# Kernel optimization log

Hardware: AMD Instinct MI355X
Metric: run time of the kernel (lower is better)

The kernel has to match this reference:

```python
import jax, jax.numpy as jnp
import numpy as np


def setup_inputs() -> dict:
    key = jax.random.key(0)
    k1, k2 = jax.random.split(key, 2)
    B, N, D = 8, 2048, 1024
    x = jax.random.normal(k1, (B, N, D), dtype=jnp.float32)
    # Linear(D, 3D): weight stored as [in, out] for x @ W
    W_qkv = jax.random.normal(k2, (D, 3 * D), dtype=jnp.float32) * (D ** -0.5)
    b_qkv = jnp.zeros((3 * D,), dtype=jnp.float32)
    return {"x": x, "W_qkv": W_qkv, "b_qkv": b_qkv}


def reference(x, W_qkv, b_qkv):
    D = x.shape[-1]
    scale = D ** -0.5
    qkv = x @ W_qkv + b_qkv                      # [B, N, 3D]
    q, k, v = jnp.split(qkv, 3, axis=-1)         # each [B, N, D]
    # attention scores: note original scales AFTER matmul (same math)
    atten = jnp.einsum('bnd,bmd->bnm', q, k) * scale  # [B, N, N]
    atten = jax.nn.softmax(atten, axis=-1)
    out = jnp.einsum('bnm,bmd->bnd', atten, v)   # [B, N, D]
    return out
```

## Files before the change

### kernel.cpp

```cpp
#include <hip/hip_runtime.h>
#include <hip/hip_bf16.h>


typedef __attribute__((ext_vector_type(8))) short bf16x8;
typedef __attribute__((ext_vector_type(4))) float f32x4;
typedef __attribute__((ext_vector_type(8))) unsigned short u16x8;
typedef __attribute__((address_space(1))) const unsigned int gu32;
typedef __attribute__((address_space(3))) unsigned int lu32;

__device__ __forceinline__ unsigned short f2bf(float f) {
  union { float f; unsigned int u; } v; v.f = f;
  unsigned int r = v.u + 0x7fffu + ((v.u >> 16) & 1u);
  return (unsigned short)(r >> 16);
}
__device__ __forceinline__ void cp16(const unsigned short* g, unsigned short* l) {
  __builtin_amdgcn_global_load_lds((gu32*)g, (lu32*)l, 16, 0, 0);
}

__global__ __launch_bounds__(256) void prep(const float* __restrict__ x,
                                            unsigned short* __restrict__ xb,
                                            const float* __restrict__ W,
                                            unsigned short* __restrict__ Wt,
                                            float* __restrict__ rowsum) {
  __shared__ unsigned short tile[64][72];
  int bid = blockIdx.x, t = threadIdx.x;
  if (bid < 8192) {
    long i = ((long)bid * 256 + t) * 8;
    float4 a = *(const float4*)(x + i);
    float4 b = *(const float4*)(x + i + 4);
    u16x8 o;
    o[0] = f2bf(a.x); o[1] = f2bf(a.y); o[2] = f2bf(a.z); o[3] = f2bf(a.w);
    o[4] = f2bf(b.x); o[5] = f2bf(b.y); o[6] = f2bf(b.z); o[7] = f2bf(b.w);
    *(u16x8*)(xb + i) = o;
  } else if (bid < 8960) {
    int wb = bid - 8192;
    int fb = wb % 48, db = wb / 48;
#pragma unroll
    for (int it = 0; it < 4; it++) {
      int c = t + it * 256;
      int r = c >> 4, c4 = (c & 15) * 4;
      float4 v = *(const float4*)(W + (long)(db * 64 + r) * 3072 + fb * 64 + c4);
      tile[r][c4 + 0] = f2bf(v.x); tile[r][c4 + 1] = f2bf(v.y);
      tile[r][c4 + 2] = f2bf(v.z); tile[r][c4 + 3] = f2bf(v.w);
    }
    __syncthreads();
#pragma unroll
    for (int it = 0; it < 2; it++) {
      int c = t + it * 256;
      int r2 = c >> 3, k8 = (c & 7) * 8;
      u16x8 o;
#pragma unroll
      for (int j = 0; j < 8; j++) o[j] = tile[k8 + j][r2];
      *(u16x8*)(Wt + (long)(fb * 64 + r2) * 1024 + db * 64 + k8) = o;
    }
  } else {
    rowsum[(bid - 8960) * 256 + t] = 0.f;
  }
}

template <int MODE, int SWZ>
__global__ __launch_bounds__(512, 2) void gemm256(
    const unsigned short* __restrict__ A, const unsigned short* __restrict__ B,
    float* __restrict__ C, const float* __restrict__ bias, int Ncols, int K, float scale,
    unsigned short* __restrict__ qp, unsigned short* __restrict__ kp,
    unsigned short* __restrict__ vp, float* __restrict__ rsum,
    long strA, long strB, long strC) {
  __shared__ __align__(16) unsigned short As[2][256 * 64];
  __shared__ __align__(16) unsigned short Bs[2][256 * 64];
  const int tid = threadIdx.x;
  const int lane = tid & 63, wave = tid >> 6;
  const int quad = lane >> 4, l16 = lane & 15;
  const int lr = lane >> 3, lc = lane & 7;
  const int bz = blockIdx.z;
  int mt, nt;
  if (SWZ == 0) {
    mt = blockIdx.y; nt = blockIdx.x;
  } else {
    int bid = blockIdx.x;
    int w = bid & 15, st = bid >> 4;
    constexpr int NSUP = (SWZ >= 4) ? (SWZ / 4) : 1;
    mt = (st / NSUP) * 4 + (w >> 2);
    nt = (st % NSUP) * 4 + (w & 3);
  }
  const long m0 = (long)mt * 256;
  const int n0 = nt * 256;
  const int wm128 = (wave >> 2) * 128;
  const int wn64 = (wave & 3) * 64;
  const int NT = K >> 6, mask = NT - 1;

  const unsigned short* __restrict__ Ab = A + (long)bz * strA;
  const unsigned short* __restrict__ Bb = B + (long)bz * strB;

  unsigned int aSrc[4], bSrc[4];
  int aOff[4], bOff[4];
  {
    const int auL[4] = {0, 128, 64, 192}, auH[4] = {32, 160, 96, 224};
    const int buL[4] = {0, 128, 32, 160}, buH[4] = {64, 192, 96, 224};
    const bool wlo = wave < 4;
    const int w8 = (wave & 3) * 8;
    const int sc = (lc ^ lr) * 8;
#pragma unroll
    for (int u = 0; u < 4; u++) {
      int ra = (wlo ? auL[u] : auH[u]) + w8 + lr;
      int rb = (wlo ? buL[u] : buH[u]) + w8 + lr;
      aSrc[u] = (unsigned int)(((int)m0 + ra) * K + sc);
      bSrc[u] = (unsigned int)((n0 + rb) * K + sc);
      aOff[u] = ra * 64 + lc * 8;
      bOff[u] = rb * 64 + lc * 8;
    }
  }

#define SA(u, bb, tt) cp16(Ab + aSrc[u] + (tt) * 64, &As[bb][aOff[u]])
#define SB(u, bb, tt) cp16(Bb + bSrc[u] + (tt) * 64, &Bs[bb][bOff[u]])

  f32x4 acc[8][4];
  f32x4 zero = {0.f, 0.f, 0.f, 0.f};
#pragma unroll
  for (int i = 0; i < 8; i++)
#pragma unroll
    for (int j = 0; j < 4; j++) acc[i][j] = zero;
  bf16x8 am[4][2], bn[4][2];

  SA(0, 0, 0); SA(1, 0, 0); SB(0, 0, 0); SB(1, 0, 0);
  SA(2, 0, 0); SA(3, 0, 0); SB(2, 0, 0); SB(3, 0, 0);
  SA(0, 1, 1); SA(1, 1, 1); SB(0, 1, 1); SB(1, 1, 1);
  SA(2, 1, 1); SA(3, 1, 1);
  asm volatile("s_waitcnt vmcnt(6)" ::: "memory");
  __builtin_amdgcn_s_barrier();

#define RD_A(bb, mg)                                                                        \
  _Pragma("unroll") for (int ii = 0; ii < 4; ii++) {                                        \
    int row = wm128 + ((mg) * 4 + ii) * 16 + l16;                                           \
    _Pragma("unroll") for (int h = 0; h < 2; h++)                                           \
      am[ii][h] = *(const bf16x8*)(&As[bb][row * 64 + ((((h << 2) | quad)) ^ (row & 7)) * 8]); \
  }
#define RD_B(bb, ng)                                                                        \
  _Pragma("unroll") for (int jj = 0; jj < 2; jj++) {                                        \
    int row = wn64 + ((ng) * 2 + jj) * 16 + l16;                                            \
    _Pragma("unroll") for (int h = 0; h < 2; h++)                                           \
      bn[(ng) * 2 + jj][h] = *(const bf16x8*)(&Bs[bb][row * 64 + ((((h << 2) | quad)) ^ (row & 7)) * 8]); \
  }
#define MM(mg, ng)                                                                          \
  _Pragma("unroll") for (int ii = 0; ii < 4; ii++)                                          \
    _Pragma("unroll") for (int jj = 0; jj < 2; jj++)                                        \
      _Pragma("unroll") for (int h = 0; h < 2; h++)                                         \
        acc[(mg) * 4 + ii][(ng) * 2 + jj] = __builtin_amdgcn_mfma_f32_16x16x32_bf16(        \
            am[ii][h], bn[(ng) * 2 + jj][h], acc[(mg) * 4 + ii][(ng) * 2 + jj], 0, 0, 0);
#define BARRIER __builtin_amdgcn_s_barrier()
#define LGKM0 asm volatile("s_waitcnt lgkmcnt(0)" ::: "memory")
#define PRIO1 __builtin_amdgcn_s_setprio(1)
#define PRIO0 __builtin_amdgcn_s_setprio(0)

#define TILE(bb, tt)                                                                        \
  {                                                                                         \
    const int t1_ = ((tt) + 1) & mask, t2_ = ((tt) + 2) & mask;                             \
                                          \
    RD_A(bb, 0); RD_B(bb, 0);                                                               \
    SB(2, (bb) ^ 1, t1_); SB(3, (bb) ^ 1, t1_);                                             \
    BARRIER; LGKM0; PRIO1; MM(0, 0); PRIO0; BARRIER;                                        \
                     \
    RD_B(bb, 1);                                                                            \
    SA(0, bb, t2_); SA(1, bb, t2_);                                                         \
    BARRIER; LGKM0; PRIO1; MM(0, 1); PRIO0; BARRIER;                                        \
                                     \
    RD_A(bb, 1);                                                                            \
    SB(0, bb, t2_); SB(1, bb, t2_);                                                         \
    BARRIER; LGKM0; PRIO1; MM(1, 0); PRIO0; BARRIER;                                        \
           \
    SA(2, bb, t2_); SA(3, bb, t2_);                                                         \
    BARRIER; PRIO1; MM(1, 1); PRIO0;                                                        \
    asm volatile("s_waitcnt vmcnt(6)" ::: "memory");                                        \
    BARRIER;                                                                                \
  }

#pragma unroll 1
  for (int t = 0; t < NT; t += 2) {
    TILE(0, t);
    TILE(1, t + 1);
  }

  if (MODE == 1) {
#pragma unroll
    for (int j = 0; j < 4; j++) {
      int fg = n0 + wn64 + j * 16 + l16;
      float bv = bias[fg];
      if (fg < 2048) {
        unsigned short* outp = (fg < 1024) ? qp : kp;
        int fo = fg & 1023;
#pragma unroll
        for (int i = 0; i < 8; i++)
#pragma unroll
          for (int r = 0; r < 4; r++) {
            long trow = m0 + wm128 + i * 16 + quad * 4 + r;
            outp[trow * 1024 + fo] = f2bf(acc[i][j][r] + bv);
          }
      } else {
        int d = fg - 2048;
#pragma unroll
        for (int i = 0; i < 8; i++)
#pragma unroll
          for (int r = 0; r < 4; r++) {
            long trow = m0 + wm128 + i * 16 + quad * 4 + r;
            vp[((long)(trow >> 11) * 1024 + d) * 2048 + (trow & 2047)] = f2bf(acc[i][j][r] + bv);
          }
      }
    }
  } else if (MODE == 3) {
    unsigned short* Co = qp + (long)bz * strC;
    float* rs = rsum + bz * 2048;
#pragma unroll
    for (int i = 0; i < 8; i++)
#pragma unroll
      for (int r = 0; r < 4; r++) {
        long gm = m0 + wm128 + i * 16 + quad * 4 + r;
        float psum = 0.f;
#pragma unroll
        for (int j = 0; j < 4; j++) {
          float e = __expf(acc[i][j][r] * scale);
          psum += e;
          Co[gm * Ncols + n0 + wn64 + j * 16 + l16] = f2bf(e);
        }
        psum += __shfl_xor(psum, 1);
        psum += __shfl_xor(psum, 2);
        psum += __shfl_xor(psum, 4);
        psum += __shfl_xor(psum, 8);
        if (l16 == 0) atomicAdd(rs + gm, psum);
      }
  } else {
    float* Co = C + (long)bz * strC;
    const float* rs = rsum + bz * 2048;
#pragma unroll
    for (int i = 0; i < 8; i++)
#pragma unroll
      for (int r = 0; r < 4; r++) {
        long gm = m0 + wm128 + i * 16 + quad * 4 + r;
        float inv = 1.0f / rs[gm];
#pragma unroll
        for (int j = 0; j < 4; j++)
          Co[gm * Ncols + n0 + wn64 + j * 16 + l16] = acc[i][j][r] * inv;
      }
  }
  asm volatile("s_waitcnt vmcnt(0)" ::: "memory");
#undef SA
#undef SB
#undef RD_A
#undef RD_B
#undef MM
#undef TILE
#undef BARRIER
#undef LGKM0
#undef PRIO1
#undef PRIO0
}

extern "C" void kernel_launch(void* const* d_in, const int* in_sizes, int n_in,
                              void* d_out, int out_size, void* d_ws, size_t ws_size,
                              hipStream_t stream) {
  const float* x = (const float*)d_in[0];
  const float* W = (const float*)d_in[1];
  const float* bq = (const float*)d_in[2];
  float* out = (float*)d_out;
  char* ws = (char*)d_ws;
  const long MB = 1L << 20;
  unsigned short* Q  = (unsigned short*)(ws);
  unsigned short* Kb = (unsigned short*)(ws + 32 * MB);
  unsigned short* Vt = (unsigned short*)(ws + 64 * MB);
  unsigned short* xb = (unsigned short*)(ws + 96 * MB);
  unsigned short* Wt = (unsigned short*)(ws + 128 * MB);
  unsigned short* E  = (unsigned short*)(ws + 96 * MB);
  float* rowsum      = (float*)(ws + 160 * MB);

  prep<<<9024, 256, 0, stream>>>(x, xb, W, Wt, rowsum);
  gemm256<1, 12><<<dim3(768, 1, 1), 512, 0, stream>>>(xb, Wt, nullptr, bq, 3072, 1024, 1.0f,
                                                      Q, Kb, Vt, nullptr, 0, 0, 0);
  gemm256<3, 8><<<dim3(64, 1, 8), 512, 0, stream>>>(Q, Kb, nullptr, nullptr, 2048, 1024,
                                                    0.03125f, E, nullptr, nullptr, rowsum,
                                                    2048L * 1024, 2048L * 1024, 2048L * 2048);
  gemm256<4, 4><<<dim3(32, 1, 8), 512, 0, stream>>>(E, Vt, out, nullptr, 1024, 2048, 1.0f,
                                                    nullptr, nullptr, nullptr, rowsum,
                                                    2048L * 2048, 1024L * 2048, 2048L * 1024);
}
```

Before: 390.3 us.

## Restructure GEMM main loop with register double-buffered A fragments and fewer barriers

Rewrites the per-tile schedule of the bf16 MFMA GEMM so that A fragments are read in quarter blocks into a double-buffered register array while the previous quarter's MFMAs run. All B fragments are loaded once per tile, and the first fragments of the next LDS buffer are prefetched before the tile ends. Each phase now uses one barrier instead of two, and global-to-LDS prefetches are issued for both halves of the next-next tile. This aims to hide LDS read latency and cut barrier stalls, at the cost of more registers and subtler LDS hazard ordering.

After: 381.9 us. 1.02x faster.

```diff
diff --git a/kernel.cpp b/kernel.cpp
--- a/kernel.cpp
+++ b/kernel.cpp
@@ -119,59 +119,64 @@
   for (int i = 0; i < 8; i++)
 #pragma unroll
     for (int j = 0; j < 4; j++) acc[i][j] = zero;
-  bf16x8 am[4][2], bn[4][2];
+  bf16x8 am[2][2][2];
+  bf16x8 bn[4][2];
+
+#define RD_AQ(d, bb, q)                                                                     \
+  _Pragma("unroll") for (int ii = 0; ii < 2; ii++) {                                        \
+    int row = wm128 + ((q) * 2 + ii) * 16 + l16;                                            \
+    _Pragma("unroll") for (int h = 0; h < 2; h++)                                           \
+      am[d][ii][h] = *(const bf16x8*)(&As[bb][row * 64 + ((((h << 2) | quad)) ^ (row & 7)) * 8]); \
+  }
+#define RD_BALL(bb)                                                                         \
+  _Pragma("unroll") for (int jj = 0; jj < 4; jj++) {                                        \
+    int row = wn64 + jj * 16 + l16;                                                         \
+    _Pragma("unroll") for (int h = 0; h < 2; h++)                                           \
+      bn[jj][h] = *(const bf16x8*)(&Bs[bb][row * 64 + ((((h << 2) | quad)) ^ (row & 7)) * 8]); \
+  }
+#define MMQ(q, d)                                                                           \
+  _Pragma("unroll") for (int ii = 0; ii < 2; ii++)                                          \
+    _Pragma("unroll") for (int jj = 0; jj < 4; jj++)                                        \
+      _Pragma("unroll") for (int h = 0; h < 2; h++)                                         \
+        acc[(q) * 2 + ii][jj] = __builtin_amdgcn_mfma_f32_16x16x32_bf16(                    \
+            am[d][ii][h], bn[jj][h], acc[(q) * 2 + ii][jj], 0, 0, 0);
+#define ABAR asm volatile("s_barrier" ::: "memory")
+#define LGKM0 asm volatile("s_waitcnt lgkmcnt(0)" ::: "memory")
+#define VMCNT4 asm volatile("s_waitcnt vmcnt(4)" ::: "memory")
+#define PRIO1 __builtin_amdgcn_s_setprio(1)
+#define PRIO0 __builtin_amdgcn_s_setprio(0)
+
+#define TILE(bb, tt)                                                                        \
+  {                                                                                         \
+    const int t2_ = ((tt) + 2) & mask;                                                      \
+                                                                                    \
+    LGKM0; RD_AQ(1, bb, 1); ABAR;                                                           \
+    SB(0, bb, t2_); SB(1, bb, t2_);                                                         \
+    PRIO1; MMQ(0, 0); PRIO0;                                                                \
+                                                                                    \
+    LGKM0; RD_AQ(0, bb, 2); ABAR;                                                           \
+    SA(0, bb, t2_); SA(1, bb, t2_);                                                         \
+    PRIO1; MMQ(1, 1); PRIO0;                                                                \
+                                                                                    \
+    LGKM0; RD_AQ(1, bb, 3); VMCNT4; ABAR;                                                   \
+    SB(2, bb, t2_); SB(3, bb, t2_);                                                         \
+    PRIO1; MMQ(2, 0); PRIO0;                                                                \
+                                                                                    \
+    LGKM0; RD_AQ(0, (bb) ^ 1, 0);                                                           \
+    PRIO1; MMQ(3, 1); PRIO0;                                                                \
+    RD_BALL((bb) ^ 1);                                                                      \
+    ABAR;                                                                                   \
+    SA(2, bb, t2_); SA(3, bb, t2_);                                                         \
+  }
 
   SA(0, 0, 0); SA(1, 0, 0); SB(0, 0, 0); SB(1, 0, 0);
   SA(2, 0, 0); SA(3, 0, 0); SB(2, 0, 0); SB(3, 0, 0);
   SA(0, 1, 1); SA(1, 1, 1); SB(0, 1, 1); SB(1, 1, 1);
-  SA(2, 1, 1); SA(3, 1, 1);
-  asm volatile("s_waitcnt vmcnt(6)" ::: "memory");
-  __builtin_amdgcn_s_barrier();
-
-#define RD_A(bb, mg)                                                                        \
-  _Pragma("unroll") for (int ii = 0; ii < 4; ii++) {                                        \
-    int row = wm128 + ((mg) * 4 + ii) * 16 + l16;                                           \
-    _Pragma("unroll") for (int h = 0; h < 2; h++)                                           \
-      am[ii][h] = *(const bf16x8*)(&As[bb][row * 64 + ((((h << 2) | quad)) ^ (row & 7)) * 8]); \
-  }
-#define RD_B(bb, ng)                                                                        \
-  _Pragma("unroll") for (int jj = 0; jj < 2; jj++) {                                        \
-    int row = wn64 + ((ng) * 2 + jj) * 16 + l16;                                            \
-    _Pragma("unroll") for (int h = 0; h < 2; h++)                                           \
-      bn[(ng) * 2 + jj][h] = *(const bf16x8*)(&Bs[bb][row * 64 + ((((h << 2) | quad)) ^ (row & 7)) * 8]); \
-  }
-#define MM(mg, ng)                                                                          \
-  _Pragma("unroll") for (int ii = 0; ii < 4; ii++)                                          \
-    _Pragma("unroll") for (int jj = 0; jj < 2; jj++)                                        \
-      _Pragma("unroll") for (int h = 0; h < 2; h++)                                         \
-        acc[(mg) * 4 + ii][(ng) * 2 + jj] = __builtin_amdgcn_mfma_f32_16x16x32_bf16(        \
-            am[ii][h], bn[(ng) * 2 + jj][h], acc[(mg) * 4 + ii][(ng) * 2 + jj], 0, 0, 0);
-#define BARRIER __builtin_amdgcn_s_barrier()
-#define LGKM0 asm volatile("s_waitcnt lgkmcnt(0)" ::: "memory")
-#define PRIO1 __builtin_amdgcn_s_setprio(1)
-#define PRIO0 __builtin_amdgcn_s_setprio(0)
-
-#define TILE(bb, tt)                                                                        \
-  {                                                                                         \
-    const int t1_ = ((tt) + 1) & mask, t2_ = ((tt) + 2) & mask;                             \
-                                          \
-    RD_A(bb, 0); RD_B(bb, 0);                                                               \
-    SB(2, (bb) ^ 1, t1_); SB(3, (bb) ^ 1, t1_);                                             \
-    BARRIER; LGKM0; PRIO1; MM(0, 0); PRIO0; BARRIER;                                        \
-                     \
-    RD_B(bb, 1);                                                                            \
-    SA(0, bb, t2_); SA(1, bb, t2_);                                                         \
-    BARRIER; LGKM0; PRIO1; MM(0, 1); PRIO0; BARRIER;                                        \
-                                     \
-    RD_A(bb, 1);                                                                            \
-    SB(0, bb, t2_); SB(1, bb, t2_);                                                         \
-    BARRIER; LGKM0; PRIO1; MM(1, 0); PRIO0; BARRIER;                                        \
-           \
-    SA(2, bb, t2_); SA(3, bb, t2_);                                                         \
-    BARRIER; PRIO1; MM(1, 1); PRIO0;                                                        \
-    asm volatile("s_waitcnt vmcnt(6)" ::: "memory");                                        \
-    BARRIER;                                                                                \
-  }
+  SA(2, 1, 1); SA(3, 1, 1); SB(2, 1, 1); SB(3, 1, 1);
+  asm volatile("s_waitcnt vmcnt(8)" ::: "memory");
+  ABAR;
+  RD_AQ(0, 0, 0);
+  RD_BALL(0);
 
 #pragma unroll 1
   for (int t = 0; t < NT; t += 2) {
@@ -240,15 +245,16 @@
           Co[gm * Ncols + n0 + wn64 + j * 16 + l16] = acc[i][j][r] * inv;
       }
   }
-  asm volatile("s_waitcnt vmcnt(0)" ::: "memory");
+  asm volatile("s_waitcnt vmcnt(0) lgkmcnt(0)" ::: "memory");
 #undef SA
 #undef SB
-#undef RD_A
-#undef RD_B
-#undef MM
+#undef RD_AQ
+#undef RD_BALL
+#undef MMQ
 #undef TILE
-#undef BARRIER
+#undef ABAR
 #undef LGKM0
+#undef VMCNT4
 #undef PRIO1
 #undef PRIO0
 }
```
